# Kernel optimization log

Hardware: AMD Instinct MI355X
Metric: run time of the kernel (lower is better)

Reference implementation:

```python
import jax, jax.numpy as jnp
import numpy as np

N = 8192
EPS = 1e-8
RADIUS2 = 0.05 ** 2  # squared neighborhood radius


def setup_inputs() -> dict:
    key = jax.random.key(0)
    ks = jax.random.split(key, 6)
    points = jax.random.uniform(ks[0], (N, 3), dtype=jnp.float32)
    seg_probs = jax.random.uniform(ks[1], (N, 3), dtype=jnp.float32)
    boundary_mask = jax.random.randint(ks[2], (N,), 0, 2) > 0
    head_mask = jax.random.randint(ks[3], (N,), 0, 2) > 0
    pred_mask = jax.random.randint(ks[4], (N,), 0, 2) > 0
    gt_mask = jax.random.randint(ks[5], (N,), 0, 2) > 0
    return {"points": points, "seg_probs": seg_probs,
            "boundary_mask": boundary_mask, "head_mask": head_mask,
            "pred_mask": pred_mask, "gt_mask": gt_mask}


def _ellipsoid_shape_loss(points, mask):
    # masked mean / covariance over head-region points, then eigen ratios
    m = mask.astype(points.dtype)[:, None]  # [N,1]
    n = jnp.sum(m)
    center = jnp.sum(points * m, axis=0) / n
    centered = (points - center) * m  # zero out non-head rows
    cov = centered.T @ centered / n  # [3,3]
    w = jnp.linalg.eigvalsh(cov)  # ascending
    a, b, c = w[2], w[1], w[0]  # descending
    loss = (b / (a + EPS) - 1.0) ** 2 + (c / (a + EPS) - 1.0) ** 2
    return jnp.where(n >= 10, loss, 0.0)


def _size_consistency_loss(pred_mask, gt_mask):
    pv = jnp.sum(pred_mask.astype(jnp.float32))
    gv = jnp.sum(gt_mask.astype(jnp.float32))
    volume_loss = (pv - gv) ** 2
    rel = jnp.abs(pv - gv) / jnp.where(gv > 0, gv, 1.0)
    return jnp.where(gv > 0, volume_loss + 0.5 * rel, volume_loss)


def _surface_smoothness_loss(points, bmask, seg_probs):
    # fused pairwise-distance + masked unbiased variance (replaces O(N) python loop)
    bf = bmask.astype(points.dtype)
    x = seg_probs[:, 2]  # head probability channel
    sq = jnp.sum(points * points, axis=1)  # [N]
    d2 = sq[:, None] + sq[None, :] - 2.0 * (points @ points.T)  # [N,N] squared dists
    vf = (d2 < RADIUS2).astype(points.dtype) * bf[:, None] * bf[None, :]  # valid pairs
    cnt = jnp.sum(vf, axis=1)  # neighbors per boundary point (incl. self)
    sx = vf @ x
    sx2 = vf @ (x * x)
    safe_n = jnp.maximum(cnt, 2.0)
    var = (sx2 - sx * sx / safe_n) / (safe_n - 1.0)  # unbiased, matches torch.var
    include = (cnt > 1.0) & bmask
    ni = jnp.sum(include)
    mean_var = jnp.sum(jnp.where(include, var, 0.0)) / jnp.maximum(ni, 1)
    ok = (jnp.sum(bf) >= 5) & (ni > 0)
    return jnp.where(ok, mean_var, 0.0)


def _connectivity_loss(points, hmask):
    hf = hmask.astype(points.dtype)
    n = jnp.sum(hf)
    center = jnp.sum(points * hf[:, None], axis=0) / n
    d = jnp.linalg.norm(points - center, axis=1)
    mean_d = jnp.sum(d * hf) / n
    var = jnp.sum(hf * (d - mean_d) ** 2) / (n - 1.0)  # unbiased
    maxd = jnp.max(jnp.where(hmask, d, -jnp.inf))
    return jnp.where(n >= 5, var / (maxd + EPS), 0.0)


def reference(points, seg_probs, boundary_mask, head_mask, pred_mask, gt_mask):
    total = (_ellipsoid_shape_loss(points, head_mask)
             + _size_consistency_loss(pred_mask, gt_mask)
             + _surface_smoothness_loss(points, boundary_mask, seg_probs)
             + _connectivity_loss(points, head_mask))
    return total
```

## Files before the change

### kernel.cpp

```cpp
#include <hip/hip_runtime.h>

#define EPSF 1e-8f
#define R2C  0.0025f
#define NJ   32


__device__ inline int read_mask(const void* p, int i, int isInt) {
    if (isInt) return ((const int*)p)[i] != 0;
    return ((const unsigned char*)p)[i] != 0;
}
__device__ inline float wave_sum(float v) {
    #pragma unroll
    for (int o = 32; o > 0; o >>= 1) v += __shfl_down(v, o, 64);
    return v;
}
__device__ inline float wave_max(float v) {
    #pragma unroll
    for (int o = 32; o > 0; o >>= 1) v = fmaxf(v, __shfl_down(v, o, 64));
    return v;
}

__global__ __launch_bounds__(256, 4)
void k_pairs(const float* __restrict__ pts, const float* __restrict__ segp,
             const void* bm, const void* hm, const void* pm, const void* gm,
             float* __restrict__ ws, int n, int nbi) {
    __shared__ float4 t4[256];
    __shared__ float2 tv[256];
    __shared__ int bad[4];
    __shared__ float pacc[8];
    int tid = threadIdx.x, lane = tid & 63;
    int bx = blockIdx.x, c = blockIdx.y;

    if (tid < 4) bad[tid] = 0;
    if (tid < 8) pacc[tid] = 0.f;
    __syncthreads();
    {
        const void* ms[4] = {bm, hm, pm, gm};
        #pragma unroll
        for (int m = 0; m < 4; ++m) {
            unsigned w = ((const unsigned*)ms[m])[tid & 255];
            if (w & 0xFFFFFF00u) atomicOr(&bad[m], 1);
        }
    }
    __syncthreads();

    int i = bx*256 + tid;
    int ic = min(i, n-1);
    bool act = i < n;
    float x = pts[3*ic], y = pts[3*ic+1], z = pts[3*ic+2];
    int b = read_mask(bm, ic, !bad[0]) && act;
    float sq = x*x + y*y + z*z;
    float sqi = b ? sq : sq + 1000.f;

    if (c == 0) {
        int h = read_mask(hm, ic, !bad[1]) && act;
        int p = read_mask(pm, ic, !bad[2]) && act;
        int g = read_mask(gm, ic, !bad[3]) && act;
        float hf = h ? 1.f : 0.f;
        float vals[7] = { hf*x, hf*y, hf*z, hf, (float)p, (float)g, (float)b };
        #pragma unroll
        for (int k = 0; k < 7; ++k) {
            float s = wave_sum(vals[k]);
            if (lane == 0) atomicAdd(&pacc[k], s);
        }
        __syncthreads();
        if (tid < 7) ws[64 + bx*8 + tid] = pacc[tid];
    }

    float* __restrict__ outb = ws + 4096;
    float ci = 0.f, s1 = 0.f, s2 = 0.f;
    for (int t = c; t < nbi; t += NJ) {
        int j = t*256 + tid;
        int jc = min(j, n-1);
        bool jact = j < n;
        float xj = pts[3*jc], yj = pts[3*jc+1], zj = pts[3*jc+2];
        int bj = read_mask(bm, jc, !bad[0]) && jact;
        float v = segp[3*jc+2];
        float sqj = xj*xj + yj*yj + zj*zj;
        __syncthreads();
        t4[tid] = make_float4(-2.f*xj, -2.f*yj, -2.f*zj, bj ? sqj : sqj + 1000.f);
        tv[tid] = make_float2(v, v*v);
        __syncthreads();
        #pragma unroll 8
        for (int k = 0; k < 256; ++k) {
            float4 pj = t4[k];
            float2 vv = tv[k];
            float acc = fmaf(pj.x, x, pj.w);
            acc = fmaf(pj.y, y, acc);
            acc = fmaf(pj.z, z, acc);
            float d2 = acc + sqi;
            float m = (d2 < R2C) ? 1.f : 0.f;
            ci += m;
            s1 = fmaf(m, vv.x, s1);
            s2 = fmaf(m, vv.y, s2);
        }
    }
    if (act) {
        outb[(size_t)c*n + i]          = ci;
        outb[(size_t)(NJ + c)*n + i]   = s1;
        outb[(size_t)(2*NJ + c)*n + i] = s2;
    }
}

__global__ void k_final(const float* __restrict__ pts, const void* bm, const void* hm,
                        float* __restrict__ ws, float* __restrict__ out, int n, int nbi) {
    __shared__ int badb, badh, lastf, bmax;
    __shared__ float ctr[8];
    __shared__ float bacc[12];
    int tid = threadIdx.x, lane = tid & 63;
    if (tid == 0) { badb = 0; badh = 0; lastf = 0; bmax = 0; }
    if (tid < 12) bacc[tid] = 0.f;
    __syncthreads();
    unsigned wb = ((const unsigned*)bm)[tid & 255];
    unsigned wh = ((const unsigned*)hm)[tid & 255];
    if (wb & 0xFFFFFF00u) atomicOr(&badb, 1);
    if (wh & 0xFFFFFF00u) atomicOr(&badh, 1);

    if (tid < 64) {
        float s[7] = {0.f,0.f,0.f,0.f,0.f,0.f,0.f};
        for (int r = tid; r < nbi; r += 64)
            #pragma unroll
            for (int k = 0; k < 7; ++k) s[k] += ws[64 + r*8 + k];
        #pragma unroll
        for (int k = 0; k < 7; ++k) {
            #pragma unroll
            for (int o = 32; o > 0; o >>= 1) s[k] += __shfl_down(s[k], o, 64);
        }
        if (tid == 0) {
            #pragma unroll
            for (int k = 0; k < 7; ++k) ctr[k] = s[k];
        }
    }
    __syncthreads();

    float nh = ctr[3];
    float inv = (nh > 0.f) ? 1.f/nh : 0.f;
    float cx = ctr[0]*inv, cy = ctr[1]*inv, cz = ctr[2]*inv;
    int i = blockIdx.x*256 + tid;
    int ic = min(i, n-1);
    float act = (i < n) ? 1.f : 0.f;
    float x = pts[3*ic], y = pts[3*ic+1], z = pts[3*ic+2];
    int h = read_mask(hm, ic, !badh);
    float m = (h ? 1.f : 0.f) * act;
    float dx = x-cx, dy = y-cy, dz = z-cz;
    float d = sqrtf(dx*dx + dy*dy + dz*dz);
    float vals[8] = { m*dx*dx, m*dx*dy, m*dx*dz, m*dy*dy, m*dy*dz, m*dz*dz,
                      m*d, m*d*d };
    #pragma unroll
    for (int k = 0; k < 8; ++k) {
        float s = wave_sum(vals[k]);
        if (lane == 0) atomicAdd(&bacc[k], s);
    }
    float dm = wave_max(m > 0.f ? d : 0.f);
    if (lane == 0) atomicMax(&bmax, __float_as_int(dm));

    const float* __restrict__ outb = ws + 4096;
    float sv = 0.f, nv = 0.f;
    if (i < n) {
        float c0 = 0.f, a1 = 0.f, a2 = 0.f;
        #pragma unroll
        for (int k = 0; k < NJ; ++k) {
            c0 += outb[(size_t)k*n + i];
            a1 += outb[(size_t)(NJ + k)*n + i];
            a2 += outb[(size_t)(2*NJ + k)*n + i];
        }
        int b = read_mask(bm, i, !badb);
        float safe_n = fmaxf(c0, 2.f);
        float var = (a2 - a1*a1/safe_n) / (safe_n - 1.f);
        if (b && c0 > 1.f) { sv = var; nv = 1.f; }
    }
    sv = wave_sum(sv); nv = wave_sum(nv);
    if (lane == 0) { atomicAdd(&bacc[9], sv); atomicAdd(&bacc[10], nv); }
    __syncthreads();

    float* row = ws + 1024 + blockIdx.x*16;
    if (tid < 12) {
        float val = (tid == 8) ? __int_as_float(bmax) : bacc[tid];
        atomicExch((int*)&row[tid], __float_as_int(val));
    }
    if (tid == 0) {
        __threadfence();
        unsigned prev = atomicAdd((unsigned*)ws, 1u);
        if (prev % (unsigned)gridDim.x == (unsigned)gridDim.x - 1u) lastf = 1;
    }
    __syncthreads();
    if (!lastf) return;

    if (tid < 12) bacc[tid] = 0.f;
    if (tid == 0) bmax = 0;
    __syncthreads();
    for (int t = tid; t < nbi*12; t += 256) {
        int r = t / 12, col = t % 12;
        int bits = atomicOr((int*)&ws[1024 + r*16 + col], 0);
        if (col == 8) atomicMax(&bmax, bits);
        else          atomicAdd(&bacc[col], __int_as_float(bits));
    }
    __syncthreads();
    if (tid != 0) return;

    float cxx=bacc[0], cxy=bacc[1], cxz=bacc[2];
    float cyy=bacc[3], cyz=bacc[4], czz=bacc[5];
    float sd=bacc[6], sd2=bacc[7], svv=bacc[9], niv=bacc[10];
    float maxd = __int_as_float(bmax);
    float pv = ctr[4], gv = ctr[5], nbm = ctr[6];

    float el = 0.0f;
    if (nh >= 10.0f) {
        double nn  = (double)nh;
        double axx = cxx/nn, axy = cxy/nn, axz = cxz/nn;
        double ayy = cyy/nn, ayz = cyz/nn, azz = czz/nn;
        double p1 = axy*axy + axz*axz + ayz*ayz;
        double q  = (axx + ayy + azz) / 3.0;
        double p2 = (axx-q)*(axx-q) + (ayy-q)*(ayy-q) + (azz-q)*(azz-q) + 2.0*p1;
        double e0, e2;
        if (p2 < 1e-300) { e0 = e2 = q; }
        else {
            double p = sqrt(p2 / 6.0);
            double bxx = (axx-q)/p, byy = (ayy-q)/p, bzz = (azz-q)/p;
            double bxy = axy/p, bxz = axz/p, byz = ayz/p;
            double detB = bxx*(byy*bzz - byz*byz) - bxy*(bxy*bzz - byz*bxz)
                        + bxz*(bxy*byz - byy*bxz);
            double r2 = fmin(1.0, fmax(-1.0, detB * 0.5));
            double phi = acos(r2) / 3.0;
            e2 = q + 2.0*p*cos(phi);
            e0 = q + 2.0*p*cos(phi + 2.0943951023931953);
        }
        double e1 = 3.0*q - e2 - e0;
        double ra = e1/(e2 + (double)EPSF) - 1.0;
        double rc = e0/(e2 + (double)EPSF) - 1.0;
        el = (float)(ra*ra + rc*rc);
    }
    float diff = pv - gv;
    float vol = diff * diff;
    float rel = fabsf(diff) / (gv > 0.0f ? gv : 1.0f);
    float sc = (gv > 0.0f) ? vol + 0.5f*rel : vol;
    float mean_var = svv / fmaxf(niv, 1.0f);
    float ss = ((nbm >= 5.0f) && (niv > 0.0f)) ? mean_var : 0.0f;
    float conn = 0.0f;
    if (nh >= 5.0f) {
        float var = (sd2 - sd*sd/nh) / (nh - 1.0f);
        conn = var / (maxd + EPSF);
    }
    out[0] = el + sc + ss + conn;
}

extern "C" void kernel_launch(void* const* d_in, const int* in_sizes, int n_in,
                              void* d_out, int out_size, void* d_ws, size_t ws_size,
                              hipStream_t stream) {
    const float* points = (const float*)d_in[0];
    const float* segp   = (const float*)d_in[1];
    const void*  bmask  = d_in[2];
    const void*  hmask  = d_in[3];
    const void*  pmask  = d_in[4];
    const void*  gmask  = d_in[5];
    float* ws  = (float*)d_ws;
    float* out = (float*)d_out;
    int n = in_sizes[2];
    int nbi = (n + 255) / 256;

    k_pairs<<<dim3(nbi, NJ), 256, 0, stream>>>(points, segp, bmask, hmask,
                                               pmask, gmask, ws, n, nbi);
    k_final<<<nbi, 256, 0, stream>>>(points, bmask, hmask, ws, out, n, nbi);
}
```

Measured before the change: 31.38 us.

## Register-block two query points per thread and fold distance threshold

```diff
diff --git a/kernel.cpp b/kernel.cpp
--- a/kernel.cpp
+++ b/kernel.cpp
@@ -44,20 +44,27 @@
     }
     __syncthreads();
 
-    int i = bx*256 + tid;
-    int ic = min(i, n-1);
-    bool act = i < n;
-    float x = pts[3*ic], y = pts[3*ic+1], z = pts[3*ic+2];
-    int b = read_mask(bm, ic, !bad[0]) && act;
-    float sq = x*x + y*y + z*z;
-    float sqi = b ? sq : sq + 1000.f;
+    int i0 = bx*512 + tid, i1 = i0 + 256;
+    int ic0 = min(i0, n-1), ic1 = min(i1, n-1);
+    bool a0 = i0 < n, a1 = i1 < n;
+    float x0 = pts[3*ic0], y0 = pts[3*ic0+1], z0 = pts[3*ic0+2];
+    float x1 = pts[3*ic1], y1 = pts[3*ic1+1], z1 = pts[3*ic1+2];
+    int b0 = read_mask(bm, ic0, !bad[0]) && a0;
+    int b1 = read_mask(bm, ic1, !bad[0]) && a1;
+    float thr0 = b0 ? R2C - (x0*x0 + y0*y0 + z0*z0) : -1e30f;
+    float thr1 = b1 ? R2C - (x1*x1 + y1*y1 + z1*z1) : -1e30f;
 
     if (c == 0) {
-        int h = read_mask(hm, ic, !bad[1]) && act;
-        int p = read_mask(pm, ic, !bad[2]) && act;
-        int g = read_mask(gm, ic, !bad[3]) && act;
-        float hf = h ? 1.f : 0.f;
-        float vals[7] = { hf*x, hf*y, hf*z, hf, (float)p, (float)g, (float)b };
+        int h0 = read_mask(hm, ic0, !bad[1]) && a0;
+        int h1 = read_mask(hm, ic1, !bad[1]) && a1;
+        int p0 = read_mask(pm, ic0, !bad[2]) && a0;
+        int p1 = read_mask(pm, ic1, !bad[2]) && a1;
+        int g0 = read_mask(gm, ic0, !bad[3]) && a0;
+        int g1 = read_mask(gm, ic1, !bad[3]) && a1;
+        float hf0 = h0 ? 1.f : 0.f, hf1 = h1 ? 1.f : 0.f;
+        float vals[7] = { hf0*x0 + hf1*x1, hf0*y0 + hf1*y1, hf0*z0 + hf1*z1,
+                          hf0 + hf1, (float)(p0 + p1), (float)(g0 + g1),
+                          (float)(b0 + b1) };
         #pragma unroll
         for (int k = 0; k < 7; ++k) {
             float s = wave_sum(vals[k]);
@@ -67,43 +74,56 @@
         if (tid < 7) ws[64 + bx*8 + tid] = pacc[tid];
     }
 
-    float* __restrict__ outb = ws + 4096;
-    float ci = 0.f, s1 = 0.f, s2 = 0.f;
-    for (int t = c; t < nbi; t += NJ) {
-        int j = t*256 + tid;
+    {
+        int j = c*256 + tid;
         int jc = min(j, n-1);
         bool jact = j < n;
         float xj = pts[3*jc], yj = pts[3*jc+1], zj = pts[3*jc+2];
         int bj = read_mask(bm, jc, !bad[0]) && jact;
         float v = segp[3*jc+2];
         float sqj = xj*xj + yj*yj + zj*zj;
-        __syncthreads();
         t4[tid] = make_float4(-2.f*xj, -2.f*yj, -2.f*zj, bj ? sqj : sqj + 1000.f);
         tv[tid] = make_float2(v, v*v);
-        __syncthreads();
-        #pragma unroll 8
-        for (int k = 0; k < 256; ++k) {
-            float4 pj = t4[k];
-            float2 vv = tv[k];
-            float acc = fmaf(pj.x, x, pj.w);
-            acc = fmaf(pj.y, y, acc);
-            acc = fmaf(pj.z, z, acc);
-            float d2 = acc + sqi;
-            float m = (d2 < R2C) ? 1.f : 0.f;
-            ci += m;
-            s1 = fmaf(m, vv.x, s1);
-            s2 = fmaf(m, vv.y, s2);
-        }
-    }
-    if (act) {
-        outb[(size_t)c*n + i]          = ci;
-        outb[(size_t)(NJ + c)*n + i]   = s1;
-        outb[(size_t)(2*NJ + c)*n + i] = s2;
+    }
+    __syncthreads();
+
+    float c0a = 0.f, s10 = 0.f, s20 = 0.f;
+    float c1a = 0.f, s11 = 0.f, s21 = 0.f;
+    #pragma unroll 8
+    for (int k = 0; k < 256; ++k) {
+        float4 pj = t4[k];
+        float2 vv = tv[k];
+        float t0 = fmaf(pj.x, x0, pj.w);
+        t0 = fmaf(pj.y, y0, t0);
+        t0 = fmaf(pj.z, z0, t0);
+        float m0 = (t0 < thr0) ? 1.f : 0.f;
+        c0a += m0;
+        s10 = fmaf(m0, vv.x, s10);
+        s20 = fmaf(m0, vv.y, s20);
+        float t1 = fmaf(pj.x, x1, pj.w);
+        t1 = fmaf(pj.y, y1, t1);
+        t1 = fmaf(pj.z, z1, t1);
+        float m1 = (t1 < thr1) ? 1.f : 0.f;
+        c1a += m1;
+        s11 = fmaf(m1, vv.x, s11);
+        s21 = fmaf(m1, vv.y, s21);
+    }
+    float* __restrict__ outb = ws + 4096;
+    if (a0) {
+        outb[(size_t)c*n + i0]          = c0a;
+        outb[(size_t)(NJ + c)*n + i0]   = s10;
+        outb[(size_t)(2*NJ + c)*n + i0] = s20;
+    }
+    if (a1) {
+        outb[(size_t)c*n + i1]          = c1a;
+        outb[(size_t)(NJ + c)*n + i1]   = s11;
+        outb[(size_t)(2*NJ + c)*n + i1] = s21;
     }
 }
 
 __global__ void k_final(const float* __restrict__ pts, const void* bm, const void* hm,
-                        float* __restrict__ ws, float* __restrict__ out, int n, int nbi) {
+                        float* __restrict__ ws, float* __restrict__ out,
+                        int n, int nbi, int nsl) {
     __shared__ int badb, badh, lastf, bmax;
     __shared__ float ctr[8];
     __shared__ float bacc[12];
@@ -118,7 +138,7 @@
 
     if (tid < 64) {
         float s[7] = {0.f,0.f,0.f,0.f,0.f,0.f,0.f};
-        for (int r = tid; r < nbi; r += 64)
+        for (int r = tid; r < nsl; r += 64)
             #pragma unroll
             for (int k = 0; k < 7; ++k) s[k] += ws[64 + r*8 + k];
         #pragma unroll
@@ -257,8 +277,9 @@
     float* out = (float*)d_out;
     int n = in_sizes[2];
     int nbi = (n + 255) / 256;
-
-    k_pairs<<<dim3(nbi, NJ), 256, 0, stream>>>(points, segp, bmask, hmask,
+    int nsl = (n + 511) / 512;
+
+    k_pairs<<<dim3(nsl, NJ), 256, 0, stream>>>(points, segp, bmask, hmask,
                                                pmask, gmask, ws, n, nbi);
-    k_final<<<nbi, 256, 0, stream>>>(points, bmask, hmask, ws, out, n, nbi);
-}
+    k_final<<<nbi, 256, 0, stream>>>(points, bmask, hmask, ws, out, n, nbi, nsl);
+}
```

Result: slower. 32.45 us (+3.4%).
